# Optimization experiments

Hardware: AMD Instinct MI355X
Metric: run time of the kernel (lower is better)

## Reference

```python
import jax, jax.numpy as jnp
import numpy as np

EPS = 1e-8  # torch.nn.CosineSimilarity default eps

B, N, C, H, W = 256, 5, 640, 10, 10
OC, OH, OW = 32, 5, 5  # AdaptiveAvgPool3d output (input_dim, 5, 5)


def _pool(v):
    # Adaptive avg pool over last 3 dims (C,H,W) -> (OC,OH,OW).
    # Exact block-mean since C%OC==0, H%OH==0, W%OW==0.
    lead = v.shape[:-3]
    v = v.reshape(lead + (OC, C // OC, OH, H // OH, OW, W // OW))
    return v.mean(axis=(-5, -3, -1))


def setup_inputs() -> dict:
    key = jax.random.key(0)
    x = jax.random.normal(key, (B, N, C, H, W), dtype=jnp.float32)
    return {"x": x}


def reference(x) -> jnp.ndarray:
    b, n = x.shape[0], x.shape[1]
    # proxy: pool of the sum over shots -> [B, OC*OH*OW]
    proxy = _pool(x.sum(axis=1)).reshape(b, -1)
    # per-shot pooled features -> [B, N, OC*OH*OW]
    feats = _pool(x).reshape(b, n, -1)
    # cosine similarity (torch formula: dot / max(||a||*||b||, eps))
    dot = jnp.einsum('bnd,bd->bn', feats, proxy)
    na = jnp.linalg.norm(feats, axis=-1)          # [B, N]
    nb = jnp.linalg.norm(proxy, axis=-1)[:, None]  # [B, 1]
    sim = dot / jnp.maximum(na * nb, EPS)          # [B, N]
    # weighted sum of raw shot features -> [B, C, H, W]
    out = jnp.einsum('bn,bnchw->bchw', sim, x)
    return out
```

## Files before the change

### kernel.cpp

```cpp
#include <hip/hip_runtime.h>

#define BB 256
#define NN 5
#define CHW 64000
#define DD 800
#define EPSF 1e-8f

typedef float f4 __attribute__((ext_vector_type(4)));

__global__ __launch_bounds__(256) void k_pool(const float* __restrict__ x,
                                              float* __restrict__ feats) {
    const int g = blockIdx.x * 256 + threadIdx.x;
    const int b = g / 800;
    const int r = g - b * 800;
    const int n = r / 160;
    const int q = r - n * 160;
    const int oc = q / 5;
    const int oh = q - oc * 5;
    const f4* __restrict__ p = reinterpret_cast<const f4*>(x) +
                               ((size_t)b * NN + n) * (CHW / 4) + oc * 500 + oh * 5;
    float s0 = 0.f, s1 = 0.f, s2 = 0.f, s3 = 0.f, s4 = 0.f;
    #pragma unroll 4
    for (int cc = 0; cc < 20; ++cc) {
        const f4 v0 = p[cc * 25 + 0];
        const f4 v1 = p[cc * 25 + 1];
        const f4 v2 = p[cc * 25 + 2];
        const f4 v3 = p[cc * 25 + 3];
        const f4 v4 = p[cc * 25 + 4];
        s0 += (v0.x + v0.y) + (v2.z + v2.w);
        s1 += (v0.z + v0.w) + (v3.x + v3.y);
        s2 += (v1.x + v1.y) + (v3.z + v3.w);
        s3 += (v1.z + v1.w) + (v4.x + v4.y);
        s4 += (v2.x + v2.y) + (v4.z + v4.w);
    }
    float* fp = feats + ((size_t)b * NN + n) * DD + oc * 25 + oh * 5;
    fp[0] = s0 * (1.f / 80.f);
    fp[1] = s1 * (1.f / 80.f);
    fp[2] = s2 * (1.f / 80.f);
    fp[3] = s3 * (1.f / 80.f);
    fp[4] = s4 * (1.f / 80.f);
}

__global__ __launch_bounds__(64) void k_sim(const float* __restrict__ feats,
                                            float* __restrict__ sim) {
    const int b = blockIdx.x;
    const int lane = threadIdx.x;
    const float* __restrict__ fb = feats + (size_t)b * NN * DD;
    float dot[NN] = {0.f, 0.f, 0.f, 0.f, 0.f};
    float na2[NN] = {0.f, 0.f, 0.f, 0.f, 0.f};
    float nb2 = 0.f;
    for (int d = lane; d < DD; d += 64) {
        float f[NN];
        float p = 0.f;
        #pragma unroll
        for (int n = 0; n < NN; ++n) { f[n] = fb[n * DD + d]; p += f[n]; }
        #pragma unroll
        for (int n = 0; n < NN; ++n) {
            dot[n] += f[n] * p;
            na2[n] += f[n] * f[n];
        }
        nb2 += p * p;
    }
    #pragma unroll
    for (int off = 32; off >= 1; off >>= 1) {
        #pragma unroll
        for (int n = 0; n < NN; ++n) {
            dot[n] += __shfl_down(dot[n], off, 64);
            na2[n] += __shfl_down(na2[n], off, 64);
        }
        nb2 += __shfl_down(nb2, off, 64);
    }
    if (lane == 0) {
        const float nb = sqrtf(nb2);
        #pragma unroll
        for (int n = 0; n < NN; ++n) {
            const float denom = fmaxf(sqrtf(na2[n]) * nb, EPSF);
            sim[b * NN + n] = dot[n] / denom;
        }
    }
}

__global__ __launch_bounds__(256) void k_out(const float* __restrict__ x,
                                             const float* __restrict__ sim,
                                             float* __restrict__ out) {
    const int i = blockIdx.x * 256 + threadIdx.x;
    const int b = (BB - 1) - i / 16000;
    const int r = i - ((BB - 1) - b) * 16000;
    const f4* __restrict__ xp =
        reinterpret_cast<const f4*>(x) + (size_t)b * (NN * 16000) + r;
    const float s0 = sim[b * NN + 0];
    const float s1 = sim[b * NN + 1];
    const float s2 = sim[b * NN + 2];
    const float s3 = sim[b * NN + 3];
    const float s4 = sim[b * NN + 4];
    const f4 a0 = xp[0 * 16000];
    const f4 a1 = xp[1 * 16000];
    const f4 a2 = xp[2 * 16000];
    const f4 a3 = xp[3 * 16000];
    const f4 a4 = xp[4 * 16000];
    f4 o = s0 * a0 + s1 * a1 + s2 * a2 + s3 * a3 + s4 * a4;
    __builtin_nontemporal_store(
        o, reinterpret_cast<f4*>(out) + (size_t)b * 16000 + r);
}

extern "C" void kernel_launch(void* const* d_in, const int* in_sizes, int n_in,
                              void* d_out, int out_size, void* d_ws, size_t ws_size,
                              hipStream_t stream) {
    const float* x = (const float*)d_in[0];
    float* out = (float*)d_out;
    float* feats = (float*)d_ws;
    float* sim = feats + (size_t)BB * NN * DD;

    k_pool<<<BB * NN * 160 / 256, 256, 0, stream>>>(x, feats);
    k_sim<<<BB, 64, 0, stream>>>(feats, sim);
    k_out<<<BB * 16000 / 256, 256, 0, stream>>>(x, sim, out);
}
```

Before: 125.1 us.

## Fuse pooling and cosine-similarity kernels into one per-batch block kernel

Merges the pooling kernel and the similarity kernel into a single kernel with one 1024-thread block per batch. The pooled features are kept in shared memory instead of going to global workspace, and the dot products and norms are reduced across the block's wavefronts. This is meant to remove one kernel launch and the global write and read of the pooled features. The risk is coarser work distribution: only 800 of 1024 threads do the pooling loads, spread over just 256 large blocks, which may lower memory-level parallelism in the bandwidth-bound pooling pass.

```diff
diff --git a/kernel.cpp b/kernel.cpp
--- a/kernel.cpp
+++ b/kernel.cpp
@@ -8,74 +8,78 @@
 
 typedef float f4 __attribute__((ext_vector_type(4)));
 
-__global__ __launch_bounds__(256) void k_pool(const float* __restrict__ x,
-                                              float* __restrict__ feats) {
-    const int g = blockIdx.x * 256 + threadIdx.x;
-    const int b = g / 800;
-    const int r = g - b * 800;
-    const int n = r / 160;
-    const int q = r - n * 160;
-    const int oc = q / 5;
-    const int oh = q - oc * 5;
-    const f4* __restrict__ p = reinterpret_cast<const f4*>(x) +
-                               ((size_t)b * NN + n) * (CHW / 4) + oc * 500 + oh * 5;
-    float s0 = 0.f, s1 = 0.f, s2 = 0.f, s3 = 0.f, s4 = 0.f;
-    #pragma unroll 4
-    for (int cc = 0; cc < 20; ++cc) {
-        const f4 v0 = p[cc * 25 + 0];
-        const f4 v1 = p[cc * 25 + 1];
-        const f4 v2 = p[cc * 25 + 2];
-        const f4 v3 = p[cc * 25 + 3];
-        const f4 v4 = p[cc * 25 + 4];
-        s0 += (v0.x + v0.y) + (v2.z + v2.w);
-        s1 += (v0.z + v0.w) + (v3.x + v3.y);
-        s2 += (v1.x + v1.y) + (v3.z + v3.w);
-        s3 += (v1.z + v1.w) + (v4.x + v4.y);
-        s4 += (v2.x + v2.y) + (v4.z + v4.w);
+__global__ __launch_bounds__(1024, 4) void k_poolsim(const float* __restrict__ x,
+                                                     float* __restrict__ sim) {
+    __shared__ float fl[NN * DD];
+    __shared__ float red[17][11];
+    const int tid = threadIdx.x;
+    const int b = blockIdx.x;
+
+    if (tid < NN * 160) {
+        const int n  = tid / 160;
+        const int r  = tid - n * 160;
+        const int oc = r / 5;
+        const int oh = r - oc * 5;
+        const f4* __restrict__ p = reinterpret_cast<const f4*>(x) +
+                                   ((size_t)b * NN + n) * (CHW / 4) + oc * 500 + oh * 5;
+        float s0 = 0.f, s1 = 0.f, s2 = 0.f, s3 = 0.f, s4 = 0.f;
+        #pragma unroll 4
+        for (int cc = 0; cc < 20; ++cc) {
+            const f4 v0 = p[cc * 25 + 0];
+            const f4 v1 = p[cc * 25 + 1];
+            const f4 v2 = p[cc * 25 + 2];
+            const f4 v3 = p[cc * 25 + 3];
+            const f4 v4 = p[cc * 25 + 4];
+            s0 += (v0.x + v0.y) + (v2.z + v2.w);
+            s1 += (v0.z + v0.w) + (v3.x + v3.y);
+            s2 += (v1.x + v1.y) + (v3.z + v3.w);
+            s3 += (v1.z + v1.w) + (v4.x + v4.y);
+            s4 += (v2.x + v2.y) + (v4.z + v4.w);
+        }
+        float* fp = fl + n * DD + oc * 25 + oh * 5;
+        fp[0] = s0 * (1.f / 80.f);
+        fp[1] = s1 * (1.f / 80.f);
+        fp[2] = s2 * (1.f / 80.f);
+        fp[3] = s3 * (1.f / 80.f);
+        fp[4] = s4 * (1.f / 80.f);
     }
-    float* fp = feats + ((size_t)b * NN + n) * DD + oc * 25 + oh * 5;
-    fp[0] = s0 * (1.f / 80.f);
-    fp[1] = s1 * (1.f / 80.f);
-    fp[2] = s2 * (1.f / 80.f);
-    fp[3] = s3 * (1.f / 80.f);
-    fp[4] = s4 * (1.f / 80.f);
-}
+    __syncthreads();
 
-__global__ __launch_bounds__(64) void k_sim(const float* __restrict__ feats,
-                                            float* __restrict__ sim) {
-    const int b = blockIdx.x;
-    const int lane = threadIdx.x;
-    const float* __restrict__ fb = feats + (size_t)b * NN * DD;
-    float dot[NN] = {0.f, 0.f, 0.f, 0.f, 0.f};
-    float na2[NN] = {0.f, 0.f, 0.f, 0.f, 0.f};
-    float nb2 = 0.f;
-    for (int d = lane; d < DD; d += 64) {
-        float f[NN];
-        float p = 0.f;
+    float part[11];
+    #pragma unroll
+    for (int k = 0; k < 11; ++k) part[k] = 0.f;
+    if (tid < DD) {
+        float f[NN], p = 0.f;
         #pragma unroll
-        for (int n = 0; n < NN; ++n) { f[n] = fb[n * DD + d]; p += f[n]; }
+        for (int n = 0; n < NN; ++n) { f[n] = fl[n * DD + tid]; p += f[n]; }
+        #pragma unroll
+        for (int n = 0; n < NN; ++n) { part[n] = f[n] * p; part[5 + n] = f[n] * f[n]; }
+        part[10] = p * p;
+    }
+    #pragma unroll
+    for (int off = 32; off >= 1; off >>= 1)
+        #pragma unroll
+        for (int k = 0; k < 11; ++k)
+            part[k] += __shfl_down(part[k], off, 64);
+    const int wv = tid >> 6;
+    if ((tid & 63) == 0) {
+        #pragma unroll
+        for (int k = 0; k < 11; ++k) red[wv][k] = part[k];
+    }
+    __syncthreads();
+    if (tid < 11) {
+        float s = 0.f;
+        #pragma unroll
+        for (int w = 0; w < 16; ++w) s += red[w][tid];
+        red[16][tid] = s;
+    }
+    __syncthreads();
+    if (tid == 0) {
+        const float nb = sqrtf(red[16][10]);
         #pragma unroll
         for (int n = 0; n < NN; ++n) {
-            dot[n] += f[n] * p;
-            na2[n] += f[n] * f[n];
-        }
-        nb2 += p * p;
-    }
-    #pragma unroll
-    for (int off = 32; off >= 1; off >>= 1) {
-        #pragma unroll
-        for (int n = 0; n < NN; ++n) {
-            dot[n] += __shfl_down(dot[n], off, 64);
-            na2[n] += __shfl_down(na2[n], off, 64);
-        }
-        nb2 += __shfl_down(nb2, off, 64);
-    }
-    if (lane == 0) {
-        const float nb = sqrtf(nb2);
-        #pragma unroll
-        for (int n = 0; n < NN; ++n) {
-            const float denom = fmaxf(sqrtf(na2[n]) * nb, EPSF);
-            sim[b * NN + n] = dot[n] / denom;
+            const float denom = fmaxf(sqrtf(red[16][5 + n]) * nb, EPSF);
+            sim[b * NN + n] = red[16][n] / denom;
         }
     }
 }
@@ -108,10 +112,8 @@
                               hipStream_t stream) {
     const float* x = (const float*)d_in[0];
     float* out = (float*)d_out;
-    float* feats = (float*)d_ws;
-    float* sim = feats + (size_t)BB * NN * DD;
+    float* sim = (float*)d_ws;
 
-    k_pool<<<BB * NN * 160 / 256, 256, 0, stream>>>(x, feats);
-    k_sim<<<BB, 64, 0, stream>>>(feats, sim);
+    k_poolsim<<<BB, 1024, 0, stream>>>(x, sim);
     k_out<<<BB * 16000 / 256, 256, 0, stream>>>(x, sim, out);
 }
```

Result: slower. 132.8 us (+6.2%).
